# Performance work log

Hardware: AMD Instinct MI355X
Metric: run time of the kernel (lower is better)

Reference implementation:

```python
import jax, jax.numpy as jnp
import numpy as np

B, C3, T = 32, 384, 2048

def setup_inputs() -> dict:
    key = jax.random.key(0)
    qkv = jax.random.normal(key, (B, C3, T), dtype=jnp.float32)
    return {"qkv": qkv}

def reference(qkv):
    # qkv: [B, 3C, T]
    ch = qkv.shape[1] // 3
    q, k, v = jnp.split(qkv, 3, axis=1)  # each [B, C, T]
    scale = 1.0 / jnp.sqrt(jnp.asarray(ch, dtype=qkv.dtype))
    # weight[b, t_q, t_k] = sum_c q[b,c,t_q] * k[b,c,t_k]
    weight = jnp.einsum('bcq,bck->bqk', q, k) * scale  # [B, T, T]
    weight = jax.nn.softmax(weight, axis=-1)
    # out[b, c, t_q] = sum_k weight[b,t_q,k] * v[b,c,k]
    out = jnp.einsum('bqk,bck->bcq', weight, v)  # [B, C, T]
    return out
```

## Files before the change

kernel.cpp:

```cpp
#include <hip/hip_runtime.h>
#include <hip/hip_bf16.h>
#include <math.h>

#define BB 32
#define CC 128
#define TT 2048
#define NCH 384

typedef __attribute__((ext_vector_type(8))) short short8;
typedef __attribute__((ext_vector_type(4))) float floatx4;

__device__ ushort g_q[(size_t)BB * TT * CC];
__device__ ushort g_k[(size_t)BB * TT * CC];
__device__ ushort g_v[(size_t)BB * CC * TT];

__device__ __forceinline__ ushort f2bf(float f) {
    uint u = __float_as_uint(f);
    u += 0x7fffu + ((u >> 16) & 1u);
    return (ushort)(u >> 16);
}

__global__ __launch_bounds__(256) void prepass_kernel(const float* __restrict__ qkv) {
    __shared__ float lds[64][133];
    const int b = blockIdx.y;
    const int t0 = blockIdx.x * 64;
    const int tid = threadIdx.x;
    const int u = tid >> 3;
    const int j = tid & 7;

    for (int part = 0; part < 2; ++part) {
        const float scale = (part == 0) ? 0.127517451f : 1.0f;
        float4 fa[4][2];
#pragma unroll
        for (int i = 0; i < 4; i++) {
            const float* src = qkv + ((size_t)(b * NCH + part * CC + i * 32 + u)) * TT + t0 + j * 8;
            fa[i][0] = *(const float4*)src;
            fa[i][1] = *(const float4*)(src + 4);
        }
        if (part) __syncthreads();
#pragma unroll
        for (int i = 0; i < 4; i++) {
            int c = i * 32 + u;
#pragma unroll
            for (int q = 0; q < 2; q++) {
                lds[j * 8 + q * 4 + 0][c] = fa[i][q].x;
                lds[j * 8 + q * 4 + 1][c] = fa[i][q].y;
                lds[j * 8 + q * 4 + 2][c] = fa[i][q].z;
                lds[j * 8 + q * 4 + 3][c] = fa[i][q].w;
            }
        }
        __syncthreads();
        ushort* dst = (part == 0 ? g_q : g_k) + ((size_t)(b * TT + t0)) * CC;
#pragma unroll
        for (int p = 0; p < 4; p++) {
            int t = p * 16 + (tid >> 4);
            int x = tid & 15;
            int cb = x ^ (t & 7);
            ushort tmp[8];
#pragma unroll
            for (int jj = 0; jj < 8; jj++) tmp[jj] = f2bf(lds[t][cb * 8 + jj] * scale);
            *(uint4*)(dst + (size_t)t * CC + x * 8) = *(uint4*)tmp;
        }
    }
    {
        const float* vsrc = qkv + ((size_t)(b * NCH + 2 * CC)) * TT + t0;
        ushort* vdst = g_v + ((size_t)(b * CC)) * TT + t0;
#pragma unroll
        for (int i = 0; i < 4; i++) {
            int idx = i * 256 + tid;
            int c = idx >> 3, db = idx & 7, sb = db ^ (c & 7);
            const float* s = vsrc + (size_t)c * TT + sb * 8;
            float4 f0 = *(const float4*)s;
            float4 f1 = *(const float4*)(s + 4);
            ushort tmp[8] = {f2bf(f0.x), f2bf(f0.y), f2bf(f0.z), f2bf(f0.w),
                             f2bf(f1.x), f2bf(f1.y), f2bf(f1.z), f2bf(f1.w)};
            *(uint4*)(vdst + (size_t)c * TT + db * 8) = *(uint4*)tmp;
        }
    }
}

__global__ __launch_bounds__(256) void attn_kernel(float* __restrict__ out) {
    __shared__ ushort Qs[64][128];
    __shared__ ushort Ks[64][128];
    __shared__ ushort Vs[128][64];
    ushort (*Ps)[16][72] = reinterpret_cast<ushort(*)[16][72]>(&Qs[0][0]);

    const int b = blockIdx.y;
    const int q0 = blockIdx.x * 64;
    const int tid = threadIdx.x;
    const int w = tid >> 6;
    const int l = tid & 63;
    const int g = l >> 4;
    const int ln = l & 15;
    const int qt_loc = (w << 4) | ln;
    const int qswz = qt_loc & 7;

    {
        const uint4* src = (const uint4*)(g_q + ((size_t)(b * TT + q0)) * CC);
        uint4* d = (uint4*)&Qs[0][0];
#pragma unroll
        for (int i = 0; i < 4; i++) d[i * 256 + tid] = src[i * 256 + tid];
    }
    __syncthreads();
    short8 qfrag[4];
#pragma unroll
    for (int ck = 0; ck < 4; ck++) {
        int cbq = (4 * ck + g) ^ qswz;
        qfrag[ck] = *(const short8*)&Qs[qt_loc][cbq * 8];
    }

    floatx4 oacc[8];
#pragma unroll
    for (int i = 0; i < 8; i++) oacc[i] = (floatx4){0.f, 0.f, 0.f, 0.f};
    float m_run = -INFINITY;
    float l_run = 0.f;

    for (int kt0 = 0; kt0 < TT; kt0 += 64) {
        __syncthreads();
        {
            const uint4* src = (const uint4*)(g_k + ((size_t)(b * TT + kt0)) * CC);
            uint4* d = (uint4*)&Ks[0][0];
#pragma unroll
            for (int i = 0; i < 4; i++) d[i * 256 + tid] = src[i * 256 + tid];
        }
        {
            const ushort* src = g_v + ((size_t)(b * CC)) * TT + kt0;
            uint4* d = (uint4*)&Vs[0][0];
#pragma unroll
            for (int i = 0; i < 4; i++) {
                int idx = i * 256 + tid;
                int c = idx >> 3, o = idx & 7;
                d[idx] = *(const uint4*)(src + (size_t)c * TT + o * 8);
            }
        }
        __syncthreads();

        floatx4 sacc[4];
#pragma unroll
        for (int s = 0; s < 4; s++) sacc[s] = (floatx4){0.f, 0.f, 0.f, 0.f};
#pragma unroll
        for (int ck = 0; ck < 4; ck++) {
#pragma unroll
            for (int s = 0; s < 4; s++) {
                int kt = 16 * s + ln;
                int cbk = (4 * ck + g) ^ (kt & 7);
                short8 ak = *(const short8*)&Ks[kt][cbk * 8];
                sacc[s] = __builtin_amdgcn_mfma_f32_16x16x32_bf16(ak, qfrag[ck], sacc[s], 0, 0, 0);
            }
        }

        float vmax = -INFINITY;
#pragma unroll
        for (int s = 0; s < 4; s++)
            vmax = fmaxf(vmax, fmaxf(fmaxf(sacc[s].x, sacc[s].y), fmaxf(sacc[s].z, sacc[s].w)));
        vmax = fmaxf(vmax, __shfl_xor(vmax, 16));
        vmax = fmaxf(vmax, __shfl_xor(vmax, 32));
        if (!__all(vmax <= m_run + 8.0f)) {
            float mnew = fmaxf(m_run, vmax);
            float alpha = exp2f(m_run - mnew);
            l_run *= alpha;
#pragma unroll
            for (int i = 0; i < 8; i++) {
                oacc[i].x *= alpha; oacc[i].y *= alpha;
                oacc[i].z *= alpha; oacc[i].w *= alpha;
            }
            m_run = mnew;
        }
        float rs = 0.f;
#pragma unroll
        for (int s = 0; s < 4; s++) {
            float p0 = exp2f(sacc[s].x - m_run);
            float p1 = exp2f(sacc[s].y - m_run);
            float p2 = exp2f(sacc[s].z - m_run);
            float p3 = exp2f(sacc[s].w - m_run);
            rs += (p0 + p1) + (p2 + p3);
            __hip_bfloat162 lo = __float22bfloat162_rn(make_float2(p0, p1));
            __hip_bfloat162 hi = __float22bfloat162_rn(make_float2(p2, p3));
            *(__hip_bfloat162*)&Ps[w][ln][16 * s + 4 * g] = lo;
            *(__hip_bfloat162*)&Ps[w][ln][16 * s + 4 * g + 2] = hi;
        }
        rs += __shfl_xor(rs, 16);
        rs += __shfl_xor(rs, 32);
        l_run += rs;

#pragma unroll
        for (int kk = 0; kk < 2; kk++) {
            short8 bp = *(const short8*)&Ps[w][ln][32 * kk + 8 * g];
#pragma unroll
            for (int ms = 0; ms < 8; ms++) {
                int c = 16 * ms + ln;
                int y = (4 * kk + g) ^ (c & 7);
                short8 av = *(const short8*)&Vs[c][y * 8];
                oacc[ms] = __builtin_amdgcn_mfma_f32_16x16x32_bf16(av, bp, oacc[ms], 0, 0, 0);
            }
        }
    }

    float inv = 1.0f / l_run;
    float* op = out + ((size_t)(b * CC)) * TT + q0 + qt_loc;
#pragma unroll
    for (int ms = 0; ms < 8; ms++) {
#pragma unroll
        for (int r = 0; r < 4; r++) {
            int c = 16 * ms + 4 * g + r;
            op[(size_t)c * TT] = oacc[ms][r] * inv;
        }
    }
}

extern "C" void kernel_launch(void* const* d_in, const int* in_sizes, int n_in,
                              void* d_out, int out_size, void* d_ws, size_t ws_size,
                              hipStream_t stream) {
    (void)in_sizes; (void)n_in; (void)d_ws; (void)ws_size; (void)out_size;
    const float* qkv = (const float*)d_in[0];
    float* out = (float*)d_out;
    dim3 grid(32, 32), blk(256);
    hipLaunchKernelGGL(prepass_kernel, grid, blk, 0, stream, qkv);
    hipLaunchKernelGGL(attn_kernel, grid, blk, 0, stream, out);
}
```

Before: 302.6 us.

## Switch attention to 32x32 MFMA with register P and double-buffered LDS-direct loads

Rewrites the attention kernel to use 32x32x16 bf16 MFMA with 128 query rows per block, up from 64. The softmax P tile stays in registers and is exchanged across half-waves with shuffles instead of going through LDS. K/V tiles are now loaded with global_load_lds into two alternating buffers, so the next tile's load overlaps with compute on the current one. The Q/K swizzle widens to 16 to match the new read pattern. The aim is higher MFMA efficiency, fewer LDS round trips and less load latency, at the cost of more registers and half as many blocks (512 blocks).

```diff
diff --git a/kernel.cpp b/kernel.cpp
--- a/kernel.cpp
+++ b/kernel.cpp
@@ -8,7 +8,7 @@
 #define NCH 384
 
 typedef __attribute__((ext_vector_type(8))) short short8;
-typedef __attribute__((ext_vector_type(4))) float floatx4;
+typedef __attribute__((ext_vector_type(16))) float floatx16;
 
 __device__ ushort g_q[(size_t)BB * TT * CC];
 __device__ ushort g_k[(size_t)BB * TT * CC];
@@ -18,6 +18,12 @@
     uint u = __float_as_uint(f);
     u += 0x7fffu + ((u >> 16) & 1u);
     return (ushort)(u >> 16);
+}
+
+typedef __attribute__((address_space(1))) const unsigned char ga_t;
+typedef __attribute__((address_space(3))) unsigned char la_t;
+__device__ __forceinline__ void glds16(const void* g, void* l) {
+    __builtin_amdgcn_global_load_lds((ga_t*)g, (la_t*)l, 16, 0, 0);
 }
 
 __global__ __launch_bounds__(256) void prepass_kernel(const float* __restrict__ qkv) {
@@ -55,7 +61,7 @@
         for (int p = 0; p < 4; p++) {
             int t = p * 16 + (tid >> 4);
             int x = tid & 15;
-            int cb = x ^ (t & 7);
+            int cb = x ^ (t & 15);
             ushort tmp[8];
 #pragma unroll
             for (int jj = 0; jj < 8; jj++) tmp[jj] = f2bf(lds[t][cb * 8 + jj] * scale);
@@ -80,132 +86,152 @@
 }
 
 __global__ __launch_bounds__(256) void attn_kernel(float* __restrict__ out) {
-    __shared__ ushort Qs[64][128];
-    __shared__ ushort Ks[64][128];
-    __shared__ ushort Vs[128][64];
-    ushort (*Ps)[16][72] = reinterpret_cast<ushort(*)[16][72]>(&Qs[0][0]);
+    __shared__ ushort smem[32768];
 
     const int b = blockIdx.y;
-    const int q0 = blockIdx.x * 64;
+    const int q0 = blockIdx.x * 128;
     const int tid = threadIdx.x;
     const int w = tid >> 6;
     const int l = tid & 63;
-    const int g = l >> 4;
-    const int ln = l & 15;
-    const int qt_loc = (w << 4) | ln;
-    const int qswz = qt_loc & 7;
-
-    {
-        const uint4* src = (const uint4*)(g_q + ((size_t)(b * TT + q0)) * CC);
-        uint4* d = (uint4*)&Qs[0][0];
-#pragma unroll
-        for (int i = 0; i < 4; i++) d[i * 256 + tid] = src[i * 256 + tid];
-    }
+    const int l31 = l & 31;
+    const int hi = l >> 5;
+    const int qrow = w * 32 + l31;
+
+    const ushort* gq = g_q + ((size_t)(b * TT + q0)) * CC;
+    const ushort* gk = g_k + ((size_t)b * TT) * CC;
+    const ushort* gv = g_v + ((size_t)b * CC) * TT;
+
+#pragma unroll
+    for (int j = 0; j < 8; j++) {
+        int inst = 8 * w + j;
+        const ushort* src = gq + (size_t)(4 * inst + (l >> 4)) * CC + (l & 15) * 8;
+        glds16(src, smem + 16384 + inst * 512 + l * 8);
+    }
+    auto stage_kv = [&](int bufoff, int kt0) {
+#pragma unroll
+        for (int j = 0; j < 4; j++) {
+            int inst = 4 * w + j;
+            const ushort* src = gk + (size_t)(kt0 + 4 * inst + (l >> 4)) * CC + (l & 15) * 8;
+            glds16(src, smem + bufoff + inst * 512 + l * 8);
+        }
+#pragma unroll
+        for (int j = 0; j < 4; j++) {
+            int inst = 4 * w + j;
+            const ushort* src = gv + (size_t)(8 * inst + (l >> 3)) * TT + kt0 + (l & 7) * 8;
+            glds16(src, smem + bufoff + 8192 + inst * 512 + l * 8);
+        }
+    };
+    stage_kv(0, 0);
     __syncthreads();
-    short8 qfrag[4];
-#pragma unroll
-    for (int ck = 0; ck < 4; ck++) {
-        int cbq = (4 * ck + g) ^ qswz;
-        qfrag[ck] = *(const short8*)&Qs[qt_loc][cbq * 8];
-    }
-
-    floatx4 oacc[8];
-#pragma unroll
-    for (int i = 0; i < 8; i++) oacc[i] = (floatx4){0.f, 0.f, 0.f, 0.f};
+
+    short8 qf[8];
+#pragma unroll
+    for (int ck = 0; ck < 8; ck++) {
+        int x = (2 * ck + hi) ^ (qrow & 15);
+        qf[ck] = *(const short8*)(smem + 16384 + qrow * 128 + x * 8);
+    }
+    __syncthreads();
+
+    floatx16 oacc[4];
+#pragma unroll
+    for (int cm = 0; cm < 4; cm++)
+#pragma unroll
+        for (int r = 0; r < 16; r++) oacc[cm][r] = 0.f;
     float m_run = -INFINITY;
     float l_run = 0.f;
 
-    for (int kt0 = 0; kt0 < TT; kt0 += 64) {
-        __syncthreads();
-        {
-            const uint4* src = (const uint4*)(g_k + ((size_t)(b * TT + kt0)) * CC);
-            uint4* d = (uint4*)&Ks[0][0];
-#pragma unroll
-            for (int i = 0; i < 4; i++) d[i * 256 + tid] = src[i * 256 + tid];
-        }
-        {
-            const ushort* src = g_v + ((size_t)(b * CC)) * TT + kt0;
-            uint4* d = (uint4*)&Vs[0][0];
-#pragma unroll
-            for (int i = 0; i < 4; i++) {
-                int idx = i * 256 + tid;
-                int c = idx >> 3, o = idx & 7;
-                d[idx] = *(const uint4*)(src + (size_t)c * TT + o * 8);
-            }
-        }
-        __syncthreads();
-
-        floatx4 sacc[4];
-#pragma unroll
-        for (int s = 0; s < 4; s++) sacc[s] = (floatx4){0.f, 0.f, 0.f, 0.f};
-#pragma unroll
-        for (int ck = 0; ck < 4; ck++) {
-#pragma unroll
-            for (int s = 0; s < 4; s++) {
-                int kt = 16 * s + ln;
-                int cbk = (4 * ck + g) ^ (kt & 7);
-                short8 ak = *(const short8*)&Ks[kt][cbk * 8];
-                sacc[s] = __builtin_amdgcn_mfma_f32_16x16x32_bf16(ak, qfrag[ck], sacc[s], 0, 0, 0);
-            }
-        }
+    auto compute = [&](int bufoff) {
+        const ushort* Ksb = smem + bufoff;
+        const ushort* Vsb = smem + bufoff + 8192;
+
+        floatx16 sacc[2];
+#pragma unroll
+        for (int th = 0; th < 2; th++)
+#pragma unroll
+            for (int r = 0; r < 16; r++) sacc[th][r] = 0.f;
+#pragma unroll
+        for (int ck = 0; ck < 8; ck++)
+#pragma unroll
+            for (int th = 0; th < 2; th++) {
+                int kt = 32 * th + l31;
+                int x = (2 * ck + hi) ^ (kt & 15);
+                short8 ak = *(const short8*)(Ksb + kt * 128 + x * 8);
+                sacc[th] = __builtin_amdgcn_mfma_f32_32x32x16_bf16(ak, qf[ck], sacc[th], 0, 0, 0);
+            }
 
         float vmax = -INFINITY;
 #pragma unroll
-        for (int s = 0; s < 4; s++)
-            vmax = fmaxf(vmax, fmaxf(fmaxf(sacc[s].x, sacc[s].y), fmaxf(sacc[s].z, sacc[s].w)));
-        vmax = fmaxf(vmax, __shfl_xor(vmax, 16));
+        for (int th = 0; th < 2; th++)
+#pragma unroll
+            for (int r = 0; r < 16; r++) vmax = fmaxf(vmax, sacc[th][r]);
         vmax = fmaxf(vmax, __shfl_xor(vmax, 32));
         if (!__all(vmax <= m_run + 8.0f)) {
             float mnew = fmaxf(m_run, vmax);
             float alpha = exp2f(m_run - mnew);
             l_run *= alpha;
 #pragma unroll
-            for (int i = 0; i < 8; i++) {
-                oacc[i].x *= alpha; oacc[i].y *= alpha;
-                oacc[i].z *= alpha; oacc[i].w *= alpha;
-            }
+            for (int cm = 0; cm < 4; cm++) oacc[cm] = oacc[cm] * alpha;
             m_run = mnew;
         }
         float rs = 0.f;
 #pragma unroll
-        for (int s = 0; s < 4; s++) {
-            float p0 = exp2f(sacc[s].x - m_run);
-            float p1 = exp2f(sacc[s].y - m_run);
-            float p2 = exp2f(sacc[s].z - m_run);
-            float p3 = exp2f(sacc[s].w - m_run);
-            rs += (p0 + p1) + (p2 + p3);
-            __hip_bfloat162 lo = __float22bfloat162_rn(make_float2(p0, p1));
-            __hip_bfloat162 hi = __float22bfloat162_rn(make_float2(p2, p3));
-            *(__hip_bfloat162*)&Ps[w][ln][16 * s + 4 * g] = lo;
-            *(__hip_bfloat162*)&Ps[w][ln][16 * s + 4 * g + 2] = hi;
-        }
-        rs += __shfl_xor(rs, 16);
+        for (int th = 0; th < 2; th++)
+#pragma unroll
+            for (int r = 0; r < 16; r++) {
+                sacc[th][r] = exp2f(sacc[th][r] - m_run);
+                rs += sacc[th][r];
+            }
         rs += __shfl_xor(rs, 32);
         l_run += rs;
 
-#pragma unroll
-        for (int kk = 0; kk < 2; kk++) {
-            short8 bp = *(const short8*)&Ps[w][ln][32 * kk + 8 * g];
-#pragma unroll
-            for (int ms = 0; ms < 8; ms++) {
-                int c = 16 * ms + ln;
-                int y = (4 * kk + g) ^ (c & 7);
-                short8 av = *(const short8*)&Vs[c][y * 8];
-                oacc[ms] = __builtin_amdgcn_mfma_f32_16x16x32_bf16(av, bp, oacc[ms], 0, 0, 0);
-            }
-        }
+        uint own[2][8], xch[2][8];
+#pragma unroll
+        for (int th = 0; th < 2; th++)
+#pragma unroll
+            for (int q8 = 0; q8 < 8; q8++) {
+                __hip_bfloat162 h = __float22bfloat162_rn(
+                    make_float2(sacc[th][2 * q8], sacc[th][2 * q8 + 1]));
+                own[th][q8] = *(uint*)&h;
+                xch[th][q8] = __shfl_xor(own[th][q8], 32);
+            }
+
+#pragma unroll
+        for (int kbg = 0; kbg < 4; kbg++) {
+            int th = kbg >> 1, kb = kbg & 1;
+            union { uint u[4]; short8 s; } bu;
+            bu.u[0] = hi ? xch[th][4 * kb + 2] : own[th][4 * kb + 0];
+            bu.u[1] = hi ? xch[th][4 * kb + 3] : own[th][4 * kb + 1];
+            bu.u[2] = hi ? own[th][4 * kb + 2] : xch[th][4 * kb + 0];
+            bu.u[3] = hi ? own[th][4 * kb + 3] : xch[th][4 * kb + 1];
+#pragma unroll
+            for (int cm = 0; cm < 4; cm++) {
+                int c = 32 * cm + l31;
+                int pos = (2 * kbg + hi) ^ (c & 7);
+                short8 av = *(const short8*)(Vsb + c * 64 + pos * 8);
+                oacc[cm] = __builtin_amdgcn_mfma_f32_32x32x16_bf16(av, bu.s, oacc[cm], 0, 0, 0);
+            }
+        }
+    };
+
+#pragma unroll 1
+    for (int t = 0; t < 32; t += 2) {
+        if (t + 1 < 32) stage_kv(16384, (t + 1) * 64);
+        compute(0);
+        __syncthreads();
+        if (t + 2 < 32) stage_kv(0, (t + 2) * 64);
+        compute(16384);
+        __syncthreads();
     }
 
     float inv = 1.0f / l_run;
-    float* op = out + ((size_t)(b * CC)) * TT + q0 + qt_loc;
-#pragma unroll
-    for (int ms = 0; ms < 8; ms++) {
-#pragma unroll
-        for (int r = 0; r < 4; r++) {
-            int c = 16 * ms + 4 * g + r;
-            op[(size_t)c * TT] = oacc[ms][r] * inv;
-        }
-    }
+    float* op = out + ((size_t)b * CC) * TT + q0 + w * 32 + l31;
+#pragma unroll
+    for (int cm = 0; cm < 4; cm++)
+#pragma unroll
+        for (int r = 0; r < 16; r++) {
+            int c = 32 * cm + (r & 3) + 8 * (r >> 2) + 4 * hi;
+            op[(size_t)c * TT] = oacc[cm][r] * inv;
+        }
 }
 
 extern "C" void kernel_launch(void* const* d_in, const int* in_sizes, int n_in,
@@ -214,7 +240,6 @@
     (void)in_sizes; (void)n_in; (void)d_ws; (void)ws_size; (void)out_size;
     const float* qkv = (const float*)d_in[0];
     float* out = (float*)d_out;
-    dim3 grid(32, 32), blk(256);
-    hipLaunchKernelGGL(prepass_kernel, grid, blk, 0, stream, qkv);
-    hipLaunchKernelGGL(attn_kernel, grid, blk, 0, stream, out);
-}
+    hipLaunchKernelGGL(prepass_kernel, dim3(32, 32), dim3(256), 0, stream, qkv);
+    hipLaunchKernelGGL(attn_kernel, dim3(16, 32), dim3(256), 0, stream, out);
+}
```

New measurement: 291.1 us. 1.04x faster.
